# Kernel optimization log

Measured on AMD Instinct MI355X. Metric: run time of the kernel, lower is better.

Reference implementation:

```python
import jax, jax.numpy as jnp
import numpy as np

B, S, D, H = 2, 2048, 1024, 16
HD = D // H  # 64


def rotate_half(x):
    x1, x2 = x[..., : x.shape[-1] // 2], x[..., x.shape[-1] // 2 :]
    return jnp.concatenate((-x2, x1), axis=-1)


def setup_inputs() -> dict:
    key = jax.random.key(0)
    ks = jax.random.split(key, 8)
    return {
        "hidden_states": jax.random.normal(ks[0], (B, S, D), jnp.float32),
        "attention_bias": jax.random.normal(ks[1], (B, 1, S, S), jnp.float32),
        "cos": jax.random.uniform(ks[2], (1, S, 1, HD), jnp.float32),
        "sin": jax.random.uniform(ks[3], (1, S, 1, HD), jnp.float32),
        "Wqkv": jax.random.normal(ks[4], (D, 3 * D), jnp.float32) * (D ** -0.5),
        "bqkv": jnp.zeros((3 * D,), jnp.float32),
        "Wo": jax.random.normal(ks[5], (D, D), jnp.float32) * (D ** -0.5),
        "bo": jnp.zeros((D,), jnp.float32),
    }


def reference(hidden_states, attention_bias, cos, sin, Wqkv, bqkv, Wo, bo):
    # packed QKV projection: [B,S,D] -> [B,S,3D]
    qkv = hidden_states @ Wqkv + bqkv
    q, k, v = jnp.split(qkv, 3, axis=-1)
    # reshape to [B,S,H,HD]
    q = q.reshape(B, S, H, HD)
    k = k.reshape(B, S, H, HD)
    v = v.reshape(B, S, H, HD)
    # rotary position embedding
    q = q * cos + rotate_half(q) * sin
    k = k * cos + rotate_half(k) * sin
    # scaled dot-product attention with additive bias
    scores = jnp.einsum("bqhd,bkhd->bhqk", q, k) / jnp.sqrt(jnp.float32(HD))
    scores = scores + attention_bias
    probs = jax.nn.softmax(scores, axis=-1)
    ctx = jnp.einsum("bhqk,bkhd->bqhd", probs, v)  # [B,S,H,HD]
    ctx = ctx.reshape(B, S, D)
    return ctx @ Wo + bo
```

## Files before the change

kernel.cpp:

```cpp
#include <hip/hip_runtime.h>
#include <stdint.h>

typedef unsigned short u16;
typedef __attribute__((ext_vector_type(8))) short short8;
typedef __attribute__((ext_vector_type(4))) float f32x4;

#define DI __device__ __forceinline__

constexpr int S_LEN = 2048;
constexpr float LOG2E = 1.44269504088896f;
constexpr float SC = 0.125f * 1.44269504088896f;

DI float bf2f(u16 u) { union { uint32_t i; float f; } v; v.i = ((uint32_t)u) << 16; return v.f; }
DI u16 f2bf(float f) {
  union { float f; uint32_t i; } v; v.f = f;
  return (u16)((v.i + 0x7FFFu + ((v.i >> 16) & 1u)) >> 16);
}
DI uint32_t cvtpk(float lo, float hi) {
  uint32_t r;
  asm("v_cvt_pk_bf16_f32 %0, %1, %2" : "=v"(r) : "v"(lo), "v"(hi));
  return r;
}
DI float exp2r(float x) {
  float r;
  asm("v_exp_f32 %0, %1" : "=v"(r) : "v"(x));
  return r;
}

DI void cp16(const void* g, void* l) {
  auto gp = reinterpret_cast<const __attribute__((address_space(1))) uint32_t*>(
      reinterpret_cast<uintptr_t>(g));
  auto lp = reinterpret_cast<__attribute__((address_space(3))) uint32_t*>(
      reinterpret_cast<uintptr_t>(l));
  __builtin_amdgcn_global_load_lds(gp, lp, 16, 0, 0);
}

DI f32x4 mfma16(short8 a, short8 b, f32x4 c) {
  return __builtin_amdgcn_mfma_f32_16x16x32_bf16(a, b, c, 0, 0, 0);
}

DI int permk(int rl) {
  return ((rl >> 5) & 1) * 32 + ((rl >> 2) & 3) * 8 + ((rl >> 4) & 1) * 4 + (rl & 3);
}

__global__ __launch_bounds__(256) void k_cvt(const float* __restrict__ in,
                                             u16* __restrict__ out, int n4) {
  int i = blockIdx.x * 256 + threadIdx.x;
  if (i >= n4) return;
  float4 v = ((const float4*)in)[i];
  ushort4 o = { f2bf(v.x), f2bf(v.y), f2bf(v.z), f2bf(v.w) };
  ((ushort4*)out)[i] = o;
}

__global__ __launch_bounds__(256) void k_cvtb(const float* __restrict__ in,
                                              u16* __restrict__ out, int n4) {
  int i = blockIdx.x * 256 + threadIdx.x;
  if (i >= n4) return;
  float4 v = ((const float4*)in)[i];
  ushort4 o = { f2bf(v.x * LOG2E), f2bf(v.y * LOG2E), f2bf(v.z * LOG2E), f2bf(v.w * LOG2E) };
  ((ushort4*)out)[i] = o;
}

__global__ __launch_bounds__(256) void k_tr2(const float* __restrict__ Wqkv,
                                             u16* __restrict__ wqkvT,
                                             const float* __restrict__ Wo,
                                             u16* __restrict__ woT) {
  __shared__ float t[32][33];
  int bx = blockIdx.x;
  const float* in;
  u16* out;
  int C;
  if (bx < 96) { in = Wqkv; out = wqkvT; C = 3072; }
  else         { bx -= 96; in = Wo; out = woT; C = 1024; }
  constexpr int R = 1024;
  int tx = threadIdx.x & 31, ty = threadIdx.x >> 5;
  int c0 = bx * 32, r0 = blockIdx.y * 32;
#pragma unroll
  for (int k = 0; k < 4; k++)
    t[ty + 8 * k][tx] = in[(size_t)(r0 + ty + 8 * k) * C + c0 + tx];
  __syncthreads();
#pragma unroll
  for (int k = 0; k < 4; k++)
    out[(size_t)(c0 + ty + 8 * k) * R + r0 + tx] = f2bf(t[tx][ty + 8 * k]);
}

template <int BM, int STORE_F32, int ROPE>
__global__ __launch_bounds__(256) void k_gemm(const u16* __restrict__ A,
                                              const u16* __restrict__ Bt,
                                              const float* __restrict__ bias,
                                              void* __restrict__ Cout,
                                              const float* __restrict__ cosb,
                                              const float* __restrict__ sinb,
                                              int N, int K, int nbx) {
  constexpr int NJ = (BM == 128) ? 4 : 2;
  __shared__ u16 Al[BM * 64];
  __shared__ u16 Bl[128 * 64];
  int nwg = gridDim.x;
  int per = nwg >> 3;
  int id = blockIdx.x;
  int sid = (id & 7) * per + (id >> 3);
  int bx = sid % nbx, by = sid / nbx;
  int row0 = by * BM, col0 = bx * 128;
  int tid = threadIdx.x;
  int lane = tid & 63, wave = tid >> 6;
  int lg = lane >> 4, lc = lane & 15;
  int wroff = (BM == 128) ? (wave >> 1) * 64 : 0;
  int wcoff = (BM == 128) ? (wave & 1) * 64 : wave * 32;
  int srow = tid >> 3, sseg = tid & 7;
  int sw = (sseg ^ (srow & 7)) * 8;
  const u16* ga = A + (size_t)(row0 + srow) * K + sw;
  const u16* gb = Bt + (size_t)(col0 + srow) * K + sw;
  f32x4 acc[4][NJ] = {};
  for (int ko = 0; ko < K; ko += 64) {
#pragma unroll
    for (int p = 0; p < BM / 32; p++)
      cp16(ga + (size_t)p * 32 * K + ko, Al + tid * 8 + p * 2048);
#pragma unroll
    for (int p = 0; p < 4; p++)
      cp16(gb + (size_t)p * 32 * K + ko, Bl + tid * 8 + p * 2048);
    __syncthreads();
#pragma unroll
    for (int kk = 0; kk < 2; kk++) {
      short8 af[4], bf[NJ];
#pragma unroll
      for (int i = 0; i < 4; i++) {
        int row = wroff + i * 16 + lc;
        af[i] = *(const short8*)&Al[row * 64 + (((kk * 4 + lg) ^ (row & 7)) * 8)];
      }
#pragma unroll
      for (int j = 0; j < NJ; j++) {
        int row = wcoff + j * 16 + lc;
        bf[j] = *(const short8*)&Bl[row * 64 + (((kk * 4 + lg) ^ (row & 7)) * 8)];
      }
#pragma unroll
      for (int i = 0; i < 4; i++)
#pragma unroll
        for (int j = 0; j < NJ; j++) acc[i][j] = mfma16(af[i], bf[j], acc[i][j]);
    }
    __syncthreads();
  }
  int cbase = col0 + wcoff + lc;
  float bv[NJ];
#pragma unroll
  for (int j = 0; j < NJ; j++) bv[j] = bias[cbase + j * 16];
  bool do_rope = false;
  if constexpr (ROPE) do_rope = (col0 < 2048);
#pragma unroll
  for (int i = 0; i < 4; i++) {
    int r = row0 + wroff + i * 16 + lg * 4;
#pragma unroll
    for (int q = 0; q < 4; q++) {
      float v[NJ];
#pragma unroll
      for (int j = 0; j < NJ; j++) v[j] = acc[i][j][q] + bv[j];
      if constexpr (ROPE) {
        if (do_rope) {
          int s = (r + q) & 2047;
          const float* cb = cosb + s * 64 + lc;
          const float* sb = sinb + s * 64 + lc;
#pragma unroll
          for (int jp = 0; jp < 2; jp++) {
            float cl = cb[jp * 16], sl = sb[jp * 16];
            float ch = cb[jp * 16 + 32], sh = sb[jp * 16 + 32];
            float x1 = v[jp], x2 = v[jp + 2];
            v[jp] = x1 * cl - x2 * sl;
            v[jp + 2] = x2 * ch + x1 * sh;
          }
        }
      }
#pragma unroll
      for (int j = 0; j < NJ; j++) {
        if constexpr (STORE_F32)
          ((float*)Cout)[(size_t)(r + q) * N + cbase + j * 16] = v[j];
        else
          ((u16*)Cout)[(size_t)(r + q) * N + cbase + j * 16] = f2bf(v[j]);
      }
    }
  }
}

__global__ __launch_bounds__(256) void k_vtrans(const u16* __restrict__ qkv,
                                                u16* __restrict__ vtg) {
  __shared__ u16 Vl[64 * 66];
  int bh = blockIdx.y, b = bh >> 4, h = bh & 15;
  int s0 = blockIdx.x * 64;
  int tid = threadIdx.x;
  int r = tid >> 3, seg = tid & 7;
  const u16* src = qkv + (size_t)(b * S_LEN + s0) * 3072 + 2048 + h * 64 + seg * 8;
#pragma unroll
  for (int p = 0; p < 2; p++) {
    int s = r + 32 * p;
    short8 v = *(const short8*)(src + (size_t)s * 3072);
    const uint32_t* vw = (const uint32_t*)&v;
    uint32_t* dst = (uint32_t*)&Vl[s * 66 + seg * 8];
#pragma unroll
    for (int q = 0; q < 4; q++) dst[q] = vw[q];
  }
  __syncthreads();
  u16* out = vtg + (size_t)bh * 64 * 2048 + s0 + seg * 8;
#pragma unroll
  for (int p = 0; p < 2; p++) {
    int d = r + 32 * p;
    short8 o;
#pragma unroll
    for (int j = 0; j < 8; j++) o[j] = (short)Vl[(seg * 8 + j) * 66 + d];
    *(short8*)(out + (size_t)d * 2048) = o;
  }
}

DI float sm_pa(const f32x4 st[4], const short8* bc, short8 pa[2]) {
  float acc = 0.f;
  uint32_t w[4][2];
#pragma unroll
  for (int j = 0; j < 4; j++) {
    int base = (j & 1) * 4;
    float b0 = bf2f((u16)(j < 2 ? bc[0][base + 0] : bc[1][base + 0]));
    float b1 = bf2f((u16)(j < 2 ? bc[0][base + 1] : bc[1][base + 1]));
    float b2 = bf2f((u16)(j < 2 ? bc[0][base + 2] : bc[1][base + 2]));
    float b3 = bf2f((u16)(j < 2 ? bc[0][base + 3] : bc[1][base + 3]));
    float e0 = exp2r(st[j][0] * SC + b0);
    float e1 = exp2r(st[j][1] * SC + b1);
    float e2 = exp2r(st[j][2] * SC + b2);
    float e3 = exp2r(st[j][3] * SC + b3);
    acc += (e0 + e1) + (e2 + e3);
    w[j][0] = cvtpk(e0, e1);
    w[j][1] = cvtpk(e2, e3);
  }
  union { short8 s; uint32_t u[4]; } p0, p1;
  p0.u[0] = w[0][0]; p0.u[1] = w[0][1]; p0.u[2] = w[1][0]; p0.u[3] = w[1][1];
  p1.u[0] = w[2][0]; p1.u[1] = w[2][1]; p1.u[2] = w[3][0]; p1.u[3] = w[3][1];
  pa[0] = p0.s;
  pa[1] = p1.s;
  return acc;
}

DI void attn_store(u16* __restrict__ ctx, const f32x4 o[4], float lsumT,
                   size_t rowbase, int hcol, int lg, int lc) {
  float rinv[4];
#pragma unroll
  for (int r = 0; r < 4; r++) rinv[r] = 1.0f / __shfl(lsumT, lg * 4 + r);
#pragma unroll
  for (int j = 0; j < 4; j++)
#pragma unroll
    for (int r = 0; r < 4; r++)
      ctx[(rowbase + lg * 4 + r) * 1024 + hcol + j * 16 + lc] =
          f2bf(o[j][r] * rinv[r]);
}

__global__ __launch_bounds__(256, 2) void k_attn(const u16* __restrict__ qkv,
                                                 const u16* __restrict__ biasl2,
                                                 const u16* __restrict__ vtg,
                                                 u16* __restrict__ ctx) {
  __shared__ u16 Kl[2][4096];
  __shared__ u16 Vl[2][4096];
  constexpr int nkt = 32;
  int id = blockIdx.x;
  int idx = id >> 3;
  int bh = (id & 7) * 4 + (idx & 3);
  int qt = idx >> 2;
  int b = bh >> 4, h = bh & 15;
  int tid = threadIdx.x, lane = tid & 63, wave = tid >> 6;
  int lg = lane >> 4, lc = lane & 15;
  int q0 = qt * 128 + wave * 32;

  const u16* qb = qkv + (size_t)(b * S_LEN + q0 + lc) * 3072 + h * 64 + lg * 8;
  short8 qf[2][2];
#pragma unroll
  for (int s = 0; s < 2; s++) {
    qf[s][0] = *(const short8*)(qb + (size_t)s * 16 * 3072);
    qf[s][1] = *(const short8*)(qb + (size_t)s * 16 * 3072 + 32);
  }

  int srow = tid >> 3, sseg = tid & 7;
  const u16* kst[2];
  const u16* vst[2];
#pragma unroll
  for (int p = 0; p < 2; p++) {
    int rl = srow + 32 * p;
    int sw = (sseg ^ (rl & 7)) * 8;
    kst[p] = qkv + (size_t)(b * S_LEN + permk(rl)) * 3072 + 1024 + h * 64 + sw;
    vst[p] = vtg + (size_t)bh * 64 * 2048 + (size_t)rl * 2048 + sw;
  }

  const u16* bp0 = biasl2 + ((size_t)b * S_LEN + q0 + lc) * 2048 + lg * 8;
  const u16* bp1 = bp0 + (size_t)16 * 2048;

  f32x4 o0[4] = {}, o1[4] = {};
  float lsum0 = 0.f, lsum1 = 0.f;

#pragma unroll
  for (int p = 0; p < 2; p++) {
    cp16(kst[p], (u16*)&Kl[0][0] + p * 2048 + tid * 8);
    cp16(vst[p], (u16*)&Vl[0][0] + p * 2048 + tid * 8);
    kst[p] += (size_t)64 * 3072;
    vst[p] += 64;
  }
  short8 bA[4], bB[4];
  bA[0] = *(const short8*)bp0;
  bA[1] = *(const short8*)(bp0 + 32);
  bA[2] = *(const short8*)bp1;
  bA[3] = *(const short8*)(bp1 + 32);
  bp0 += 64;
  bp1 += 64;
  __syncthreads();

  auto tile = [&](int kt, int cur, const short8* bc, short8* bn) {
    if (kt < nkt - 1) {
#pragma unroll
      for (int p = 0; p < 2; p++) {
        cp16(kst[p], (u16*)&Kl[cur ^ 1][0] + p * 2048 + tid * 8);
        cp16(vst[p], (u16*)&Vl[cur ^ 1][0] + p * 2048 + tid * 8);
        kst[p] += (size_t)64 * 3072;
        vst[p] += 64;
      }
      bn[0] = *(const short8*)bp0;
      bn[1] = *(const short8*)(bp0 + 32);
      bn[2] = *(const short8*)bp1;
      bn[3] = *(const short8*)(bp1 + 32);
      bp0 += 64;
      bp1 += 64;
    }
    f32x4 st0[4] = {}, st1[4] = {};
    __builtin_amdgcn_s_setprio(1);
#pragma unroll
    for (int kk = 0; kk < 2; kk++) {
      short8 kf[4];
#pragma unroll
      for (int j = 0; j < 4; j++) {
        int row = j * 16 + lc;
        kf[j] = *(const short8*)&Kl[cur][row * 64 + (((kk * 4 + lg) ^ (row & 7)) * 8)];
      }
#pragma unroll
      for (int j = 0; j < 4; j++) {
        st0[j] = mfma16(kf[j], qf[0][kk], st0[j]);
        st1[j] = mfma16(kf[j], qf[1][kk], st1[j]);
      }
    }
    __builtin_amdgcn_s_setprio(0);
    short8 pa0[2], pa1[2];
    lsum0 += sm_pa(st0, bc, pa0);
    lsum1 += sm_pa(st1, bc + 2, pa1);
    __builtin_amdgcn_s_setprio(1);
#pragma unroll
    for (int kk = 0; kk < 2; kk++) {
      short8 vf[4];
#pragma unroll
      for (int j = 0; j < 4; j++) {
        int row = j * 16 + lc;
        vf[j] = *(const short8*)&Vl[cur][row * 64 + (((kk * 4 + lg) ^ (row & 7)) * 8)];
      }
#pragma unroll
      for (int j = 0; j < 4; j++) {
        o0[j] = mfma16(pa0[kk], vf[j], o0[j]);
        o1[j] = mfma16(pa1[kk], vf[j], o1[j]);
      }
    }
    __builtin_amdgcn_s_setprio(0);
    __syncthreads();
  };

  for (int kt = 0; kt < nkt; kt += 2) {
    tile(kt, 0, bA, bB);
    tile(kt + 1, 1, bB, bA);
  }

  float t0 = lsum0;
  t0 += __shfl_xor(t0, 16);
  t0 += __shfl_xor(t0, 32);
  float t1 = lsum1;
  t1 += __shfl_xor(t1, 16);
  t1 += __shfl_xor(t1, 32);
  size_t rowbase = (size_t)b * S_LEN + q0;
  attn_store(ctx, o0, t0, rowbase, h * 64, lg, lc);
  attn_store(ctx, o1, t1, rowbase + 16, h * 64, lg, lc);
}

extern "C" void kernel_launch(void* const* d_in, const int* in_sizes, int n_in,
                              void* d_out, int out_size, void* d_ws, size_t ws_size,
                              hipStream_t stream) {
  (void)in_sizes; (void)n_in; (void)out_size; (void)ws_size;
  const float* hs   = (const float*)d_in[0];
  const float* bias = (const float*)d_in[1];
  const float* cosb = (const float*)d_in[2];
  const float* sinb = (const float*)d_in[3];
  const float* Wqkv = (const float*)d_in[4];
  const float* bqkv = (const float*)d_in[5];
  const float* Wo   = (const float*)d_in[6];
  const float* bo   = (const float*)d_in[7];
  float* out = (float*)d_out;
  char* ws = (char*)d_ws;
  u16* h_bf   = (u16*)(ws + 0);
  u16* wqkvT  = (u16*)(ws + 8388608);
  u16* woT    = (u16*)(ws + 14680064);
  u16* biasbf = (u16*)(ws + 16777216);
  u16* qkv    = (u16*)(ws + 33554432);
  u16* vtg    = (u16*)(ws + 58720256);
  u16* ctxb   = (u16*)(ws + 67108864);

  k_cvt<<<4096, 256, 0, stream>>>(hs, h_bf, 1048576);
  k_cvtb<<<8192, 256, 0, stream>>>(bias, biasbf, 2097152);
  k_tr2<<<dim3(128, 32), 256, 0, stream>>>(Wqkv, wqkvT, Wo, woT);
  k_gemm<128, 0, 1><<<768, 256, 0, stream>>>(h_bf, wqkvT, bqkv, qkv, cosb, sinb,
                                             3072, 1024, 24);
  k_vtrans<<<dim3(32, 32), 256, 0, stream>>>(qkv, vtg);
  k_attn<<<512, 256, 0, stream>>>(qkv, biasbf, vtg, ctxb);
  k_gemm<64, 1, 0><<<512, 256, 0, stream>>>(ctxb, woT, bo, out, nullptr, nullptr,
                                            1024, 1024, 8);
}
```

Measured before the change: 142.4 us.

## Fuse prep conversions into one kernel and write transposed V from QKV GEMM epilogue

Merges the three preprocessing kernels (hidden-state cast, bias cast with log2e scaling, weight transposes) into a single launch that dispatches on block index. The QKV GEMM epilogue now writes V tiles directly in transposed [b,h,d,s] layout, which removes the separate V transpose kernel and its extra read and write of V. This cuts two kernel launches and one global round-trip. The trade-off is that V stores become 8-byte writes strided by 2048 elements, which may coalesce worse than before.

```diff
diff --git a/kernel.cpp b/kernel.cpp
--- a/kernel.cpp
+++ b/kernel.cpp
@@ -43,38 +43,42 @@
   return ((rl >> 5) & 1) * 32 + ((rl >> 2) & 3) * 8 + ((rl >> 4) & 1) * 4 + (rl & 3);
 }
 
-__global__ __launch_bounds__(256) void k_cvt(const float* __restrict__ in,
-                                             u16* __restrict__ out, int n4) {
-  int i = blockIdx.x * 256 + threadIdx.x;
-  if (i >= n4) return;
-  float4 v = ((const float4*)in)[i];
-  ushort4 o = { f2bf(v.x), f2bf(v.y), f2bf(v.z), f2bf(v.w) };
-  ((ushort4*)out)[i] = o;
-}
-
-__global__ __launch_bounds__(256) void k_cvtb(const float* __restrict__ in,
-                                              u16* __restrict__ out, int n4) {
-  int i = blockIdx.x * 256 + threadIdx.x;
-  if (i >= n4) return;
-  float4 v = ((const float4*)in)[i];
-  ushort4 o = { f2bf(v.x * LOG2E), f2bf(v.y * LOG2E), f2bf(v.z * LOG2E), f2bf(v.w * LOG2E) };
-  ((ushort4*)out)[i] = o;
-}
-
-__global__ __launch_bounds__(256) void k_tr2(const float* __restrict__ Wqkv,
-                                             u16* __restrict__ wqkvT,
-                                             const float* __restrict__ Wo,
-                                             u16* __restrict__ woT) {
+__global__ __launch_bounds__(256) void k_prep(const float* __restrict__ hs,
+                                              u16* __restrict__ h_bf,
+                                              const float* __restrict__ bias,
+                                              u16* __restrict__ biasbf,
+                                              const float* __restrict__ Wqkv,
+                                              u16* __restrict__ wqkvT,
+                                              const float* __restrict__ Wo,
+                                              u16* __restrict__ woT) {
+  int bid = blockIdx.x;
+  int tid = threadIdx.x;
+  if (bid < 4096) {
+    int i = bid * 256 + tid;
+    float4 v = ((const float4*)hs)[i];
+    ushort4 o = { f2bf(v.x), f2bf(v.y), f2bf(v.z), f2bf(v.w) };
+    ((ushort4*)h_bf)[i] = o;
+    return;
+  }
+  if (bid < 12288) {
+    int i = (bid - 4096) * 256 + tid;
+    float4 v = ((const float4*)bias)[i];
+    ushort4 o = { f2bf(v.x * LOG2E), f2bf(v.y * LOG2E),
+                  f2bf(v.z * LOG2E), f2bf(v.w * LOG2E) };
+    ((ushort4*)biasbf)[i] = o;
+    return;
+  }
   __shared__ float t[32][33];
-  int bx = blockIdx.x;
+  int tt = bid - 12288;
+  int bx = tt & 127, by = tt >> 7;
   const float* in;
   u16* out;
   int C;
   if (bx < 96) { in = Wqkv; out = wqkvT; C = 3072; }
   else         { bx -= 96; in = Wo; out = woT; C = 1024; }
   constexpr int R = 1024;
-  int tx = threadIdx.x & 31, ty = threadIdx.x >> 5;
-  int c0 = bx * 32, r0 = blockIdx.y * 32;
+  int tx = tid & 31, ty = tid >> 5;
+  int c0 = bx * 32, r0 = by * 32;
 #pragma unroll
   for (int k = 0; k < 4; k++)
     t[ty + 8 * k][tx] = in[(size_t)(r0 + ty + 8 * k) * C + c0 + tx];
@@ -84,11 +88,12 @@
     out[(size_t)(c0 + ty + 8 * k) * R + r0 + tx] = f2bf(t[tx][ty + 8 * k]);
 }
 
-template <int BM, int STORE_F32, int ROPE>
+template <int BM, int STORE_F32, int QKV>
 __global__ __launch_bounds__(256) void k_gemm(const u16* __restrict__ A,
                                               const u16* __restrict__ Bt,
                                               const float* __restrict__ bias,
                                               void* __restrict__ Cout,
+                                              u16* __restrict__ vtg,
                                               const float* __restrict__ cosb,
                                               const float* __restrict__ sinb,
                                               int N, int K, int nbx) {
@@ -143,8 +148,25 @@
   float bv[NJ];
 #pragma unroll
   for (int j = 0; j < NJ; j++) bv[j] = bias[cbase + j * 16];
-  bool do_rope = false;
-  if constexpr (ROPE) do_rope = (col0 < 2048);
+
+  if constexpr (QKV) {
+    if (col0 >= 2048) {
+#pragma unroll
+      for (int i = 0; i < 4; i++) {
+        int r = row0 + wroff + i * 16 + lg * 4;
+        int bq = r >> 11, s0 = r & 2047;
+#pragma unroll
+        for (int j = 0; j < NJ; j++) {
+          int c = cbase + j * 16 - 2048;
+          int h = c >> 6, d = c & 63;
+          ushort4 o4 = { f2bf(acc[i][j][0] + bv[j]), f2bf(acc[i][j][1] + bv[j]),
+                         f2bf(acc[i][j][2] + bv[j]), f2bf(acc[i][j][3] + bv[j]) };
+          *(ushort4*)&vtg[(size_t)(bq * 16 + h) * 131072 + (size_t)d * 2048 + s0] = o4;
+        }
+      }
+      return;
+    }
+  }
 #pragma unroll
   for (int i = 0; i < 4; i++) {
     int r = row0 + wroff + i * 16 + lg * 4;
@@ -153,19 +175,17 @@
       float v[NJ];
 #pragma unroll
       for (int j = 0; j < NJ; j++) v[j] = acc[i][j][q] + bv[j];
-      if constexpr (ROPE) {
-        if (do_rope) {
-          int s = (r + q) & 2047;
-          const float* cb = cosb + s * 64 + lc;
-          const float* sb = sinb + s * 64 + lc;
-#pragma unroll
-          for (int jp = 0; jp < 2; jp++) {
-            float cl = cb[jp * 16], sl = sb[jp * 16];
-            float ch = cb[jp * 16 + 32], sh = sb[jp * 16 + 32];
-            float x1 = v[jp], x2 = v[jp + 2];
-            v[jp] = x1 * cl - x2 * sl;
-            v[jp + 2] = x2 * ch + x1 * sh;
-          }
+      if constexpr (QKV) {
+        int s = (r + q) & 2047;
+        const float* cb = cosb + s * 64 + lc;
+        const float* sb = sinb + s * 64 + lc;
+#pragma unroll
+        for (int jp = 0; jp < 2; jp++) {
+          float cl = cb[jp * 16], sl = sb[jp * 16];
+          float ch = cb[jp * 16 + 32], sh = sb[jp * 16 + 32];
+          float x1 = v[jp], x2 = v[jp + 2];
+          v[jp] = x1 * cl - x2 * sl;
+          v[jp + 2] = x2 * ch + x1 * sh;
         }
       }
 #pragma unroll
@@ -176,35 +196,6 @@
           ((u16*)Cout)[(size_t)(r + q) * N + cbase + j * 16] = f2bf(v[j]);
       }
     }
-  }
-}
-
-__global__ __launch_bounds__(256) void k_vtrans(const u16* __restrict__ qkv,
-                                                u16* __restrict__ vtg) {
-  __shared__ u16 Vl[64 * 66];
-  int bh = blockIdx.y, b = bh >> 4, h = bh & 15;
-  int s0 = blockIdx.x * 64;
-  int tid = threadIdx.x;
-  int r = tid >> 3, seg = tid & 7;
-  const u16* src = qkv + (size_t)(b * S_LEN + s0) * 3072 + 2048 + h * 64 + seg * 8;
-#pragma unroll
-  for (int p = 0; p < 2; p++) {
-    int s = r + 32 * p;
-    short8 v = *(const short8*)(src + (size_t)s * 3072);
-    const uint32_t* vw = (const uint32_t*)&v;
-    uint32_t* dst = (uint32_t*)&Vl[s * 66 + seg * 8];
-#pragma unroll
-    for (int q = 0; q < 4; q++) dst[q] = vw[q];
-  }
-  __syncthreads();
-  u16* out = vtg + (size_t)bh * 64 * 2048 + s0 + seg * 8;
-#pragma unroll
-  for (int p = 0; p < 2; p++) {
-    int d = r + 32 * p;
-    short8 o;
-#pragma unroll
-    for (int j = 0; j < 8; j++) o[j] = (short)Vl[(seg * 8 + j) * 66 + d];
-    *(short8*)(out + (size_t)d * 2048) = o;
   }
 }
 
@@ -397,13 +388,10 @@
   u16* vtg    = (u16*)(ws + 58720256);
   u16* ctxb   = (u16*)(ws + 67108864);
 
-  k_cvt<<<4096, 256, 0, stream>>>(hs, h_bf, 1048576);
-  k_cvtb<<<8192, 256, 0, stream>>>(bias, biasbf, 2097152);
-  k_tr2<<<dim3(128, 32), 256, 0, stream>>>(Wqkv, wqkvT, Wo, woT);
-  k_gemm<128, 0, 1><<<768, 256, 0, stream>>>(h_bf, wqkvT, bqkv, qkv, cosb, sinb,
-                                             3072, 1024, 24);
-  k_vtrans<<<dim3(32, 32), 256, 0, stream>>>(qkv, vtg);
+  k_prep<<<16384, 256, 0, stream>>>(hs, h_bf, bias, biasbf, Wqkv, wqkvT, Wo, woT);
+  k_gemm<128, 0, 1><<<768, 256, 0, stream>>>(h_bf, wqkvT, bqkv, qkv, vtg,
+                                             cosb, sinb, 3072, 1024, 24);
   k_attn<<<512, 256, 0, stream>>>(qkv, biasbf, vtg, ctxb);
-  k_gemm<64, 1, 0><<<512, 256, 0, stream>>>(ctxb, woT, bo, out, nullptr, nullptr,
-                                            1024, 1024, 8);
-}
+  k_gemm<64, 1, 0><<<512, 256, 0, stream>>>(ctxb, woT, bo, out, nullptr,
+                                            nullptr, nullptr, 1024, 1024, 8);
+}
```

Result: no change. 140.3 us (-1.4%).
